# Kernel optimization log

Measured on AMD Instinct MI355X. Metric: run time of the kernel, lower is better.

The kernel has to match this reference:

```python
import jax, jax.numpy as jnp
import numpy as np
import math

VOCAB = 32000
DIM = 1024
TOKENS = 4096
PAD_IDX = 0
NBITS = 4
QN = -(2 ** (NBITS - 1))        # -8
QP = 2 ** (NBITS - 1) - 1       # 7


def setup_inputs() -> dict:
    key = jax.random.key(0)
    k_idx, k_w = jax.random.split(key)
    idx = jax.random.randint(k_idx, (TOKENS,), 0, VOCAB)
    # x is one-hot over the vocabulary, as implied by topk(x,1)[1] extracting the index
    x = jax.nn.one_hot(idx, VOCAB, dtype=jnp.float32)
    weight = jax.random.normal(k_w, (DIM, VOCAB), dtype=jnp.float32) * 0.02
    # LSQ init rule: alpha = 2 * mean|W| / sqrt(Qp)
    alpha = (2.0 * jnp.mean(jnp.abs(weight)) / math.sqrt(QP)).reshape(1)
    return {"x": x, "weight": weight, "alpha": alpha}


def reference(x, weight, alpha):
    # topk(x, 1)[1] on a one-hot input == argmax over vocab
    idx = jnp.argmax(x, axis=-1)                       # [T]
    mask = (idx == PAD_IDX)[:, None]                   # [T, 1]
    a = alpha[0]
    # LSQ fake-quantize the weight: round(clamp(w/alpha, Qn, Qp)) * alpha
    w_q = jnp.round(jnp.clip(weight / a, QN, QP)) * a  # [DIM, VOCAB]
    out = jnp.einsum('tv,dv->td', x, w_q)              # [T, DIM]
    return jnp.where(mask, 0.0, out)
```

## Files before the change

### kernel.cpp

```cpp
#include <hip/hip_runtime.h>


typedef float        v4f __attribute__((ext_vector_type(4)));
typedef unsigned int v4u __attribute__((ext_vector_type(4)));
typedef unsigned int u32;

constexpr int VOCAB  = 32000;
constexpr int DIM    = 1024;
constexpr int TOKENS = 4096;
constexpr int V4     = VOCAB / 4;
constexpr int WPT    = 8;
constexpr int WIN    = 64 * WPT;
constexpr int NWIN   = V4 / WIN;
constexpr int TAILB  = NWIN * WIN;
constexpr int TAILC  = (V4 - TAILB) / 64;

__device__ __forceinline__ int word_of(v4u c) {
    return c.x ? 0 : (c.y ? 1 : (c.z ? 2 : 3));
}

__global__ __launch_bounds__(256, 8) void emb_lsq_kernel(
    const float* __restrict__ x,
    const float* __restrict__ w,
    const float* __restrict__ alpha,
    float* __restrict__ out)
{
    const int lane = threadIdx.x & 63;
    const int t    = blockIdx.x * 4 + (threadIdx.x >> 6);

    const v4u* xr = reinterpret_cast<const v4u*>(x + (size_t)t * VOCAB);
    int cand = -1;
    for (int k = 0; k < NWIN; ++k) {
        const int i = lane + WIN * k;
        v4u c0 = xr[i];
        v4u c1 = xr[i +  64];
        v4u c2 = xr[i + 128];
        v4u c3 = xr[i + 192];
        v4u c4 = xr[i + 256];
        v4u c5 = xr[i + 320];
        v4u c6 = xr[i + 384];
        v4u c7 = xr[i + 448];
        u32 m0 = c0.x | c0.y | c0.z | c0.w;
        u32 m1 = c1.x | c1.y | c1.z | c1.w;
        u32 m2 = c2.x | c2.y | c2.z | c2.w;
        u32 m3 = c3.x | c3.y | c3.z | c3.w;
        u32 m4 = c4.x | c4.y | c4.z | c4.w;
        u32 m5 = c5.x | c5.y | c5.z | c5.w;
        u32 m6 = c6.x | c6.y | c6.z | c6.w;
        u32 m7 = c7.x | c7.y | c7.z | c7.w;
        if      (m0) cand = 4 * (i      ) + word_of(c0);
        else if (m1) cand = 4 * (i +  64) + word_of(c1);
        else if (m2) cand = 4 * (i + 128) + word_of(c2);
        else if (m3) cand = 4 * (i + 192) + word_of(c3);
        else if (m4) cand = 4 * (i + 256) + word_of(c4);
        else if (m5) cand = 4 * (i + 320) + word_of(c5);
        else if (m6) cand = 4 * (i + 384) + word_of(c6);
        else if (m7) cand = 4 * (i + 448) + word_of(c7);
        if (__ballot(cand >= 0)) break;
    }
    if (!__ballot(cand >= 0)) {
        #pragma unroll
        for (int j = 0; j < TAILC; ++j) {
            const int c = TAILB + lane + 64 * j;
            v4u v = xr[c];
            u32 m = v.x | v.y | v.z | v.w;
            if (cand < 0 && m) cand = 4 * c + word_of(v);
        }
    }
    const unsigned long long msk = __ballot(cand >= 0);
    const int idx = msk ? __shfl(cand, (int)__ffsll(msk) - 1) : 0;

    v4f* orow = reinterpret_cast<v4f*>(out + (size_t)t * DIM);
    if (idx <= 0) {
        v4f z = 0.f;
        #pragma unroll
        for (int j = 0; j < 4; ++j) orow[lane + 64 * j] = z;
    } else {
        const float a = alpha[0];
        const size_t col = (size_t)idx;
        float wv[16];
        #pragma unroll
        for (int j = 0; j < 4; ++j) {
            const int d0 = 4 * lane + 256 * j;
            wv[4*j+0] = w[(size_t)(d0 + 0) * VOCAB + col];
            wv[4*j+1] = w[(size_t)(d0 + 1) * VOCAB + col];
            wv[4*j+2] = w[(size_t)(d0 + 2) * VOCAB + col];
            wv[4*j+3] = w[(size_t)(d0 + 3) * VOCAB + col];
        }
        #pragma unroll
        for (int j = 0; j < 4; ++j) {
            v4f q;
            q.x = rintf(fminf(fmaxf(wv[4*j+0] / a, -8.f), 7.f)) * a;
            q.y = rintf(fminf(fmaxf(wv[4*j+1] / a, -8.f), 7.f)) * a;
            q.z = rintf(fminf(fmaxf(wv[4*j+2] / a, -8.f), 7.f)) * a;
            q.w = rintf(fminf(fmaxf(wv[4*j+3] / a, -8.f), 7.f)) * a;
            orow[lane + 64 * j] = q;
        }
    }
}

extern "C" void kernel_launch(void* const* d_in, const int* in_sizes, int n_in,
                              void* d_out, int out_size, void* d_ws, size_t ws_size,
                              hipStream_t stream) {
    const float* x     = (const float*)d_in[0];
    const float* w     = (const float*)d_in[1];
    const float* alpha = (const float*)d_in[2];
    float* out         = (float*)d_out;

    emb_lsq_kernel<<<TOKENS / 4, 256, 0, stream>>>(x, w, alpha, out);
}
```

Measured before the change: 727.2 us.

## Double-buffer one-hot row scan with prefetch, one wavefront per block

The one-hot row scan now software-pipelines its loads: the next 512-vector window is loaded into a second register buffer while the current window is tested, so the wave's early exit does not serialize on load latency. The launch changes to one 64-thread block per token instead of four wavefronts per block. This hides memory latency in the argmax search, at the cost of doubled register use and one possibly wasted window load after the hit.

Measured after the change: 729.1 us. Within noise of the previous version (+0.3%).

```diff
diff --git a/kernel.cpp b/kernel.cpp
--- a/kernel.cpp
+++ b/kernel.cpp
@@ -18,53 +18,53 @@
 __device__ __forceinline__ int word_of(v4u c) {
     return c.x ? 0 : (c.y ? 1 : (c.z ? 2 : 3));
 }
+__device__ __forceinline__ u32 nz(v4u c) { return c.x | c.y | c.z | c.w; }
 
-__global__ __launch_bounds__(256, 8) void emb_lsq_kernel(
+__global__ __launch_bounds__(64) void emb_lsq_kernel(
     const float* __restrict__ x,
     const float* __restrict__ w,
     const float* __restrict__ alpha,
     float* __restrict__ out)
 {
-    const int lane = threadIdx.x & 63;
-    const int t    = blockIdx.x * 4 + (threadIdx.x >> 6);
+    const int lane = threadIdx.x;
+    const int t    = blockIdx.x;
 
     const v4u* xr = reinterpret_cast<const v4u*>(x + (size_t)t * VOCAB);
-    int cand = -1;
+    int  cand = -1;
+    bool done = false;
+
+    v4u A[WPT], B[WPT];
+    #pragma unroll
+    for (int j = 0; j < WPT; ++j) A[j] = xr[lane + 64 * j];
+
+    #pragma unroll
     for (int k = 0; k < NWIN; ++k) {
-        const int i = lane + WIN * k;
-        v4u c0 = xr[i];
-        v4u c1 = xr[i +  64];
-        v4u c2 = xr[i + 128];
-        v4u c3 = xr[i + 192];
-        v4u c4 = xr[i + 256];
-        v4u c5 = xr[i + 320];
-        v4u c6 = xr[i + 384];
-        v4u c7 = xr[i + 448];
-        u32 m0 = c0.x | c0.y | c0.z | c0.w;
-        u32 m1 = c1.x | c1.y | c1.z | c1.w;
-        u32 m2 = c2.x | c2.y | c2.z | c2.w;
-        u32 m3 = c3.x | c3.y | c3.z | c3.w;
-        u32 m4 = c4.x | c4.y | c4.z | c4.w;
-        u32 m5 = c5.x | c5.y | c5.z | c5.w;
-        u32 m6 = c6.x | c6.y | c6.z | c6.w;
-        u32 m7 = c7.x | c7.y | c7.z | c7.w;
-        if      (m0) cand = 4 * (i      ) + word_of(c0);
-        else if (m1) cand = 4 * (i +  64) + word_of(c1);
-        else if (m2) cand = 4 * (i + 128) + word_of(c2);
-        else if (m3) cand = 4 * (i + 192) + word_of(c3);
-        else if (m4) cand = 4 * (i + 256) + word_of(c4);
-        else if (m5) cand = 4 * (i + 320) + word_of(c5);
-        else if (m6) cand = 4 * (i + 384) + word_of(c6);
-        else if (m7) cand = 4 * (i + 448) + word_of(c7);
-        if (__ballot(cand >= 0)) break;
+        if (k + 1 < NWIN) {
+            #pragma unroll
+            for (int j = 0; j < WPT; ++j)
+                B[j] = xr[(k + 1) * WIN + lane + 64 * j];
+        }
+        u32 m = 0;
+        #pragma unroll
+        for (int j = 0; j < WPT; ++j) m |= nz(A[j]);
+        if (__ballot(m != 0)) {
+            if (m) {
+                #pragma unroll
+                for (int j = 0; j < WPT; ++j)
+                    if (nz(A[j])) cand = 4 * (k * WIN + lane + 64 * j) + word_of(A[j]);
+            }
+            done = true;
+            break;
+        }
+        #pragma unroll
+        for (int j = 0; j < WPT; ++j) A[j] = B[j];
     }
-    if (!__ballot(cand >= 0)) {
+    if (!done) {
         #pragma unroll
         for (int j = 0; j < TAILC; ++j) {
             const int c = TAILB + lane + 64 * j;
             v4u v = xr[c];
-            u32 m = v.x | v.y | v.z | v.w;
-            if (cand < 0 && m) cand = 4 * c + word_of(v);
+            if (nz(v)) cand = 4 * c + word_of(v);
         }
     }
     const unsigned long long msk = __ballot(cand >= 0);
@@ -107,5 +107,5 @@
     const float* alpha = (const float*)d_in[2];
     float* out         = (float*)d_out;
 
-    emb_lsq_kernel<<<TOKENS / 4, 256, 0, stream>>>(x, w, alpha, out);
+    emb_lsq_kernel<<<TOKENS, 64, 0, stream>>>(x, w, alpha, out);
 }
```
